# Performance work log

Hardware: AMD Instinct MI355X
Metric: run time of the kernel (lower is better)

The kernel has to match this reference:

```python
import jax, jax.numpy as jnp
import numpy as np

B, D, T_STEPS = 256, 512, 256


def setup_inputs() -> dict:
    key = jax.random.key(0)
    k1, k2 = jax.random.split(key)
    # Scale K like flax lecun_normal init (std = 1/sqrt(fan_in)) so rollout stays stable.
    z0 = jax.random.normal(k1, (B, D), dtype=jnp.float32)
    K = jax.random.normal(k2, (D, D), dtype=jnp.float32) / np.sqrt(D)
    return {"z0": z0, "K": K, "T": T_STEPS}


def reference(z0, K, T):
    # z_{t+1} = z_t @ K  (flax Linear with use_bias=False: y = x @ kernel)
    def step(z, _):
        z_next = z @ K  # [B, D] @ [D, D] -> [B, D]
        return z_next, z_next

    _, preds = jax.lax.scan(step, z0, xs=None, length=T)  # [T, B, D]
    return jnp.transpose(preds, (1, 0, 2))  # [B, T, D]
```

## Files before the change

### kernel.cpp

```cpp
#include <hip/hip_runtime.h>


typedef unsigned short u16;
typedef unsigned int u32;
typedef __bf16 bf16x8 __attribute__((ext_vector_type(8)));
typedef float f32x4 __attribute__((ext_vector_type(4)));
typedef u16 u16x4 __attribute__((ext_vector_type(4)));
typedef u16 u16x8 __attribute__((ext_vector_type(8)));

#define MAT 262144
#define SLOT 1048576
#define WSLOT 131072

__device__ __forceinline__ u16 f2b(float f) {
  u32 x = __float_as_uint(f);
  return (u16)((x + 0x7fffu + ((x >> 16) & 1u)) >> 16);
}
__device__ __forceinline__ float b2f(u16 u) { return __uint_as_float(((u32)u) << 16); }

__device__ __forceinline__ size_t pidx(int r, int k) {
  return (size_t)(((r >> 4) * 16 + (k >> 5)) * 512 + ((k >> 3) & 3) * 128 + (r & 15) * 8 + (k & 7));
}

__device__ __forceinline__ void gll16(const void* g, void* l) {
  __builtin_amdgcn_global_load_lds((__attribute__((address_space(1))) void*)(void*)g,
                                   (__attribute__((address_space(3))) void*)l, 16, 0, 0);
}

__global__ __launch_bounds__(256) void prep_kernel(const float* __restrict__ Kc,
                                                   const float* __restrict__ z0,
                                                   u16* __restrict__ P,
                                                   u16* __restrict__ Uh,
                                                   u16* __restrict__ Ul) {
  int tid = threadIdx.x, b = blockIdx.x;
  if (b < 64) {
    int r0 = (b >> 3) * 64, c0b = (b & 7) * 64;
#pragma unroll
    for (int q = 0; q < 2; ++q) {
      int g = q * 256 + tid;
      int r = r0 + (g >> 3), c0 = c0b + (g & 7) * 8;
      float4 v0 = *(const float4*)(Kc + (size_t)r * 512 + c0);
      float4 v1 = *(const float4*)(Kc + (size_t)r * 512 + c0 + 4);
      float v[8] = {v0.x, v0.y, v0.z, v0.w, v1.x, v1.y, v1.z, v1.w};
      u16x8 h8, l8v;
#pragma unroll
      for (int j = 0; j < 8; ++j) {
        u16 h = f2b(v[j]);
        h8[j] = h;
        l8v[j] = f2b(v[j] - b2f(h));
        size_t ib = pidx(c0 + j, r);
        P[2 * MAT + ib] = h;
        P[3 * MAT + ib] = l8v[j];
      }
      size_t ia = pidx(r, c0);
      *(u16x8*)(P + ia) = h8;
      *(u16x8*)(P + MAT + ia) = l8v;
    }
  } else {
    int idb = b - 64;
#pragma unroll
    for (int q = 0; q < 4; ++q) {
      int g = (idb * 4 + q) * 256 + tid;
      int r = g >> 6, c0 = (g & 63) * 8;
      float4 v0 = *(const float4*)(z0 + (size_t)r * 512 + c0);
      float4 v1 = *(const float4*)(z0 + (size_t)r * 512 + c0 + 4);
      float v[8] = {v0.x, v0.y, v0.z, v0.w, v1.x, v1.y, v1.z, v1.w};
      u16x8 h8, l8v;
#pragma unroll
      for (int j = 0; j < 8; ++j) {
        u16 h = f2b(v[j]);
        h8[j] = h;
        l8v[j] = f2b(v[j] - b2f(h));
      }
      size_t ia = pidx(r, c0);
      *(u16x8*)(Uh + ia) = h8;
      *(u16x8*)(Ul + ia) = l8v;
    }
  }
}

__global__ __launch_bounds__(256, 2) void gemm_stage(
    const u16* __restrict__ fA, long fAstr,
    u16* __restrict__ fC, long fCstr,
    const u16* __restrict__ Bh, int nfull, int rowmask, int tlomask,
    const u16* __restrict__ UA, u16* __restrict__ UC) {
  __shared__ u16 Bs[32768];
  int z = blockIdx.z, y = blockIdx.y;
  const u16 *Ah, *Al;
  u16 *Ch, *Clo, *CTh, *CTl;
  int m0;
  bool full = (y < 8 * nfull);
  bool wrow, wtlo;
  if (full) {
    Ah = fA + (size_t)z * fAstr;
    Al = Ah + MAT;
    Ch = fC + (size_t)z * fCstr;
    Clo = Ch + MAT;
    CTh = Ch + 2 * MAT;
    CTl = Ch + 3 * MAT;
    m0 = y * 64;
    wrow = (rowmask >> z) & 1;
    wtlo = (tlomask >> z) & 1;
  } else {
    int yy = y - 8 * nfull;
    int u = yy >> 2;
    Ah = UA + (size_t)u * WSLOT;
    Al = Ah + 16 * (size_t)WSLOT;
    Ch = UC + (size_t)u * WSLOT;
    Clo = Ch + 16 * (size_t)WSLOT;
    CTh = CTl = nullptr;
    m0 = (yy & 3) * 64;
    wrow = true;
    wtlo = false;
  }
  const u16* Bl = Bh + MAT;
  int tid = threadIdx.x;
  int n0 = blockIdx.x * 32;
  int wv = tid >> 6, lane = tid & 63;
  int mrow = lane & 15, quad = lane >> 4;
  int l8 = lane * 8;
  int nchunk0 = n0 >> 4;
  const u16* ph = Bh + (size_t)nchunk0 * 16 * 512;
  const u16* pl = Bl + (size_t)nchunk0 * 16 * 512;
#pragma unroll
  for (int i = 0; i < 8; ++i) {
    int ch = wv * 8 + i;
    gll16(ph + (size_t)ch * 512 + l8, Bs + ch * 512);
    gll16(pl + (size_t)ch * 512 + l8, Bs + 16384 + ch * 512);
  }
  __syncthreads();
  int mc = (m0 >> 4) + wv;
  f32x4 acc[2] = {};
#pragma unroll 4
  for (int kt = 0; kt < 16; ++kt) {
    size_t co = (size_t)(mc * 16 + kt) * 512 + l8;
    bf16x8 ah = *(const bf16x8*)(Ah + co);
    bf16x8 al = *(const bf16x8*)(Al + co);
#pragma unroll
    for (int nt = 0; nt < 2; ++nt) {
      bf16x8 bh = *(const bf16x8*)(Bs + (nt * 16 + kt) * 512 + l8);
      bf16x8 bl = *(const bf16x8*)(Bs + 16384 + (nt * 16 + kt) * 512 + l8);
      acc[nt] = __builtin_amdgcn_mfma_f32_16x16x32_bf16(ah, bh, acc[nt], 0, 0, 0);
      acc[nt] = __builtin_amdgcn_mfma_f32_16x16x32_bf16(al, bh, acc[nt], 0, 0, 0);
      acc[nt] = __builtin_amdgcn_mfma_f32_16x16x32_bf16(ah, bl, acc[nt], 0, 0, 0);
    }
  }
  int mbase = m0 + wv * 16 + quad * 4;
#pragma unroll
  for (int nt = 0; nt < 2; ++nt) {
    int n = n0 + nt * 16 + mrow;
    u16x4 h4, l4;
#pragma unroll
    for (int r = 0; r < 4; ++r) {
      float v = acc[nt][r];
      u16 h = f2b(v);
      h4[r] = h;
      l4[r] = f2b(v - b2f(h));
    }
    if (wrow) {
#pragma unroll
      for (int r = 0; r < 4; ++r) {
        size_t ia = pidx(mbase + r, n);
        Ch[ia] = h4[r];
        Clo[ia] = l4[r];
      }
    }
    if (full) {
      size_t ib = pidx(n, mbase);
      *(u16x4*)(CTh + ib) = h4;
      if (wtlo) *(u16x4*)(CTl + ib) = l4;
    }
  }
}

__global__ __launch_bounds__(256, 4) void gemm_out(const u16* __restrict__ Wb,
                                                   const u16* __restrict__ PT0,
                                                   float* __restrict__ out) {
  __shared__ u16 Bs[16384];
  int z = blockIdx.z;
  const u16* A = Wb + (size_t)(z >> 4) * WSLOT;
  const u16* Bt = PT0 + (size_t)(z & 15) * SLOT;
  int tid = threadIdx.x;
  int n0 = blockIdx.x * 64;
  int wv = tid >> 6, lane = tid & 63;
  int mrow = lane & 15, quad = lane >> 4;
  int l8 = lane * 8;
  const u16* pb = Bt + (size_t)(n0 >> 4) * 16 * 512;
  int mc0 = wv * 4;
  f32x4 acc[4][4] = {};
#pragma unroll
  for (int h = 0; h < 2; ++h) {
#pragma unroll
    for (int i = 0; i < 8; ++i) {
      int c = wv * 8 + i;
      int nc = c >> 3, kc = c & 7;
      gll16(pb + (size_t)(nc * 16 + h * 8 + kc) * 512 + l8, Bs + c * 512);
    }
    __syncthreads();
#pragma unroll 4
    for (int kt = 0; kt < 8; ++kt) {
      int ktg = h * 8 + kt;
      bf16x8 a[4], b[4];
#pragma unroll
      for (int mt = 0; mt < 4; ++mt)
        a[mt] = *(const bf16x8*)(A + (size_t)((mc0 + mt) * 16 + ktg) * 512 + l8);
#pragma unroll
      for (int nt = 0; nt < 4; ++nt)
        b[nt] = *(const bf16x8*)(Bs + (nt * 8 + kt) * 512 + l8);
#pragma unroll
      for (int mt = 0; mt < 4; ++mt)
#pragma unroll
        for (int nt = 0; nt < 4; ++nt)
          acc[mt][nt] = __builtin_amdgcn_mfma_f32_16x16x32_bf16(a[mt], b[nt], acc[mt][nt], 0, 0, 0);
    }
    if (h == 0) __syncthreads();
  }
#pragma unroll
  for (int mt = 0; mt < 4; ++mt)
#pragma unroll
    for (int nt = 0; nt < 4; ++nt) {
      int gb = wv * 64 + mt * 16 + quad * 4;
      int gd = n0 + nt * 16 + mrow;
#pragma unroll
      for (int r = 0; r < 4; ++r)
        out[((size_t)(gb + r) * 256 + z) * 512 + gd] = acc[mt][nt][r];
    }
}

extern "C" void kernel_launch(void* const* d_in, const int* in_sizes, int n_in,
                              void* d_out, int out_size, void* d_ws, size_t ws_size,
                              hipStream_t stream) {
  const float* z0 = (const float*)d_in[0];
  const float* Kc = (const float*)d_in[1];
  float* out = (float*)d_out;
  u16* Uh = (u16*)d_ws;
  u16* Ul = Uh + 16 * (size_t)WSLOT;
  u16* P = Ul + 16 * (size_t)WSLOT;
  auto S = [&](int s) { return P + (size_t)s * SLOT; };
  dim3 blk(256);

  prep_kernel<<<80, blk, 0, stream>>>(Kc, z0, P, Uh, Ul);
  gemm_stage<<<dim3(16, 8, 1), blk, 0, stream>>>(S(0), 0, S(1), 0, S(0) + 2 * MAT, 1, 0x1, 0x1, nullptr, nullptr);
  gemm_stage<<<dim3(16, 8, 2), blk, 0, stream>>>(S(0), SLOT, S(2), SLOT, S(1) + 2 * MAT, 1, 0x3, 0x2, nullptr, nullptr);
  gemm_stage<<<dim3(16, 8, 4), blk, 0, stream>>>(S(0), SLOT, S(4), SLOT, S(3) + 2 * MAT, 1, 0xF, 0x8, nullptr, nullptr);
  gemm_stage<<<dim3(16, 8, 8), blk, 0, stream>>>(S(0), SLOT, S(8), SLOT, S(7) + 2 * MAT, 1, 0x80, 0x80, nullptr, nullptr);
  gemm_stage<<<dim3(16, 12, 1), blk, 0, stream>>>(S(15), 0, S(16), 0, S(15) + 2 * MAT, 1, 0x1, 0x1, Uh, Uh + 1 * (size_t)WSLOT);
  gemm_stage<<<dim3(16, 16, 1), blk, 0, stream>>>(S(16), 0, S(17), 0, S(16) + 2 * MAT, 1, 0x1, 0x1, Uh, Uh + 2 * (size_t)WSLOT);
  gemm_stage<<<dim3(16, 24, 1), blk, 0, stream>>>(S(17), 0, S(18), 0, S(17) + 2 * MAT, 1, 0x0, 0x1, Uh, Uh + 4 * (size_t)WSLOT);
  gemm_stage<<<dim3(16, 32, 1), blk, 0, stream>>>(S(18), 0, S(18), 0, S(18) + 2 * MAT, 0, 0x0, 0x0, Uh, Uh + 8 * (size_t)WSLOT);
  gemm_out<<<dim3(8, 1, 256), blk, 0, stream>>>(Uh, P + 2 * MAT, out);
}
```

Before: 240.6 us.

## Fuse output GEMM jobs into stage launches to overlap with doubling stages

Adds extra blocks to each gemm_stage launch that compute slices of the final output projection for timesteps whose ingredients are already available, so the output work overlaps with the serial matrix-power/state doubling stages. The final gemm_out launch then only handles the remaining 128 timesteps. The aim is to fill idle CUs during the small early stages and shorten the tail. The cost is larger grids and a shared-memory-heavy kernel running the output jobs at lower occupancy.

```diff
diff --git a/kernel.cpp b/kernel.cpp
--- a/kernel.cpp
+++ b/kernel.cpp
@@ -79,13 +79,67 @@
   }
 }
 
+__device__ __forceinline__ void out_job64(u16* Bs, int tid, int x, int zo,
+                                          const u16* __restrict__ Ub,
+                                          const u16* __restrict__ PT0,
+                                          float* __restrict__ out) {
+  const u16* A = Ub + (size_t)(zo >> 4) * WSLOT;
+  const u16* Bt = PT0 + (size_t)(zo & 15) * SLOT;
+  int n0 = x * 64;
+  int wv = tid >> 6, lane = tid & 63;
+  int mrow = lane & 15, quad = lane >> 4;
+  int l8 = lane * 8;
+  const u16* pb = Bt + (size_t)(n0 >> 4) * 16 * 512;
+#pragma unroll
+  for (int i = 0; i < 16; ++i) {
+    int ch = wv * 16 + i;
+    gll16(pb + (size_t)ch * 512 + l8, Bs + ch * 512);
+  }
+  __syncthreads();
+  int mc0 = wv * 4;
+  f32x4 acc[4][4] = {};
+#pragma unroll 4
+  for (int kt = 0; kt < 16; ++kt) {
+    bf16x8 a[4], b[4];
+#pragma unroll
+    for (int mt = 0; mt < 4; ++mt)
+      a[mt] = *(const bf16x8*)(A + (size_t)((mc0 + mt) * 16 + kt) * 512 + l8);
+#pragma unroll
+    for (int nt = 0; nt < 4; ++nt)
+      b[nt] = *(const bf16x8*)(Bs + (nt * 16 + kt) * 512 + l8);
+#pragma unroll
+    for (int mt = 0; mt < 4; ++mt)
+#pragma unroll
+      for (int nt = 0; nt < 4; ++nt)
+        acc[mt][nt] = __builtin_amdgcn_mfma_f32_16x16x32_bf16(a[mt], b[nt], acc[mt][nt], 0, 0, 0);
+  }
+#pragma unroll
+  for (int mt = 0; mt < 4; ++mt)
+#pragma unroll
+    for (int nt = 0; nt < 4; ++nt) {
+      int gb = wv * 64 + mt * 16 + quad * 4;
+      int gd = n0 + nt * 16 + mrow;
+#pragma unroll
+      for (int r = 0; r < 4; ++r)
+        out[((size_t)(gb + r) * 256 + zo) * 512 + gd] = acc[mt][nt][r];
+    }
+}
+
 __global__ __launch_bounds__(256, 2) void gemm_stage(
     const u16* __restrict__ fA, long fAstr,
     u16* __restrict__ fC, long fCstr,
     const u16* __restrict__ Bh, int nfull, int rowmask, int tlomask,
-    const u16* __restrict__ UA, u16* __restrict__ UC) {
+    const u16* __restrict__ UA, u16* __restrict__ UC,
+    const u16* __restrict__ PT0, float* __restrict__ out,
+    int ny0, int nout, int zbase) {
   __shared__ u16 Bs[32768];
+  int tid = threadIdx.x;
   int z = blockIdx.z, y = blockIdx.y;
+  if (y >= ny0) {
+    int e = ((y - ny0) * (int)gridDim.z + z) * 16 + (int)blockIdx.x;
+    if (e < nout) out_job64(Bs, tid, e & 7, zbase + (e >> 3), UA, PT0, out);
+    return;
+  }
   const u16 *Ah, *Al;
   u16 *Ch, *Clo, *CTh, *CTl;
   int m0;
@@ -114,7 +168,6 @@
     wtlo = false;
   }
   const u16* Bl = Bh + MAT;
-  int tid = threadIdx.x;
   int n0 = blockIdx.x * 32;
   int wv = tid >> 6, lane = tid & 63;
   int mrow = lane & 15, quad = lane >> 4;
@@ -175,9 +228,9 @@
 
 __global__ __launch_bounds__(256, 4) void gemm_out(const u16* __restrict__ Wb,
                                                    const u16* __restrict__ PT0,
-                                                   float* __restrict__ out) {
+                                                   float* __restrict__ out, int zofs) {
   __shared__ u16 Bs[16384];
-  int z = blockIdx.z;
+  int z = blockIdx.z + zofs;
   const u16* A = Wb + (size_t)(z >> 4) * WSLOT;
   const u16* Bt = PT0 + (size_t)(z & 15) * SLOT;
   int tid = threadIdx.x;
@@ -236,17 +289,18 @@
   u16* Uh = (u16*)d_ws;
   u16* Ul = Uh + 16 * (size_t)WSLOT;
   u16* P = Ul + 16 * (size_t)WSLOT;
+  u16* PT = P + 2 * MAT;
   auto S = [&](int s) { return P + (size_t)s * SLOT; };
   dim3 blk(256);
 
   prep_kernel<<<80, blk, 0, stream>>>(Kc, z0, P, Uh, Ul);
-  gemm_stage<<<dim3(16, 8, 1), blk, 0, stream>>>(S(0), 0, S(1), 0, S(0) + 2 * MAT, 1, 0x1, 0x1, nullptr, nullptr);
-  gemm_stage<<<dim3(16, 8, 2), blk, 0, stream>>>(S(0), SLOT, S(2), SLOT, S(1) + 2 * MAT, 1, 0x3, 0x2, nullptr, nullptr);
-  gemm_stage<<<dim3(16, 8, 4), blk, 0, stream>>>(S(0), SLOT, S(4), SLOT, S(3) + 2 * MAT, 1, 0xF, 0x8, nullptr, nullptr);
-  gemm_stage<<<dim3(16, 8, 8), blk, 0, stream>>>(S(0), SLOT, S(8), SLOT, S(7) + 2 * MAT, 1, 0x80, 0x80, nullptr, nullptr);
-  gemm_stage<<<dim3(16, 12, 1), blk, 0, stream>>>(S(15), 0, S(16), 0, S(15) + 2 * MAT, 1, 0x1, 0x1, Uh, Uh + 1 * (size_t)WSLOT);
-  gemm_stage<<<dim3(16, 16, 1), blk, 0, stream>>>(S(16), 0, S(17), 0, S(16) + 2 * MAT, 1, 0x1, 0x1, Uh, Uh + 2 * (size_t)WSLOT);
-  gemm_stage<<<dim3(16, 24, 1), blk, 0, stream>>>(S(17), 0, S(18), 0, S(17) + 2 * MAT, 1, 0x0, 0x1, Uh, Uh + 4 * (size_t)WSLOT);
-  gemm_stage<<<dim3(16, 32, 1), blk, 0, stream>>>(S(18), 0, S(18), 0, S(18) + 2 * MAT, 0, 0x0, 0x0, Uh, Uh + 8 * (size_t)WSLOT);
-  gemm_out<<<dim3(8, 1, 256), blk, 0, stream>>>(Uh, P + 2 * MAT, out);
-}
+  gemm_stage<<<dim3(16, 9, 1), blk, 0, stream>>>(S(0), 0, S(1), 0, S(0) + 2 * MAT, 1, 0x1, 0x1, Uh, nullptr, PT, out, 8, 8, 0);
+  gemm_stage<<<dim3(16, 9, 2), blk, 0, stream>>>(S(0), SLOT, S(2), SLOT, S(1) + 2 * MAT, 1, 0x3, 0x2, Uh, nullptr, PT, out, 8, 8, 1);
+  gemm_stage<<<dim3(16, 9, 4), blk, 0, stream>>>(S(0), SLOT, S(4), SLOT, S(3) + 2 * MAT, 1, 0xF, 0x8, Uh, nullptr, PT, out, 8, 16, 2);
+  gemm_stage<<<dim3(16, 9, 8), blk, 0, stream>>>(S(0), SLOT, S(8), SLOT, S(7) + 2 * MAT, 1, 0x80, 0x80, Uh, nullptr, PT, out, 8, 32, 4);
+  gemm_stage<<<dim3(16, 16, 1), blk, 0, stream>>>(S(15), 0, S(16), 0, S(15) + 2 * MAT, 1, 0x1, 0x1, Uh, Uh + 1 * (size_t)WSLOT, PT, out, 12, 64, 8);
+  gemm_stage<<<dim3(16, 24, 1), blk, 0, stream>>>(S(16), 0, S(17), 0, S(16) + 2 * MAT, 1, 0x1, 0x1, Uh, Uh + 2 * (size_t)WSLOT, PT, out, 16, 128, 16);
+  gemm_stage<<<dim3(16, 40, 1), blk, 0, stream>>>(S(17), 0, S(18), 0, S(17) + 2 * MAT, 1, 0x0, 0x1, Uh, Uh + 4 * (size_t)WSLOT, PT, out, 24, 256, 32);
+  gemm_stage<<<dim3(16, 64, 1), blk, 0, stream>>>(S(18), 0, S(18), 0, S(18) + 2 * MAT, 0, 0x0, 0x0, Uh, Uh + 8 * (size_t)WSLOT, PT, out, 32, 512, 64);
+  gemm_out<<<dim3(8, 1, 128), blk, 0, stream>>>(Uh, PT, out, 128);
+}
```

New measurement: 263.8 us. +9.7%, slower.
